# Kernel tuning notes

Hardware: AMD Instinct MI355X
Metric: run time of the kernel (lower is better)

The kernel has to match this reference:

```python
import jax, jax.numpy as jnp
import numpy as np

B, T, C = 16, 2048, 384
HEAD = 384

def setup_inputs() -> dict:
    key = jax.random.key(0)
    kx, kq, kk, kv = jax.random.split(key, 4)
    s = 1.0 / np.sqrt(C)
    return {
        "x": jax.random.normal(kx, (B, T, C), dtype=jnp.float32),
        "Wq": jax.random.normal(kq, (C, HEAD), dtype=jnp.float32) * s,
        "Wk": jax.random.normal(kk, (C, HEAD), dtype=jnp.float32) * s,
        "Wv": jax.random.normal(kv, (C, HEAD), dtype=jnp.float32) * s,
    }

def reference(x, Wq, Wk, Wv):
    # x: [B,T,C]; single causal attention head, eval mode (dropout = identity)
    Bc, Tc, Cc = x.shape
    q = jnp.einsum('btc,ch->bth', x, Wq)
    k = jnp.einsum('btc,ch->bth', x, Wk)
    v = jnp.einsum('btc,ch->bth', x, Wv)
    # NOTE: original scales by C**-0.5 (embedding dim), not head_size**-0.5
    scale = Cc ** (-0.5)
    wei = jnp.einsum('bth,bsh->bts', q, k) * scale  # [B,T,T]
    causal = jnp.tril(jnp.ones((Tc, Tc), dtype=bool))
    wei = jnp.where(causal, wei, -jnp.inf)
    wei = jax.nn.softmax(wei, axis=-1)
    out = jnp.einsum('bts,bsh->bth', wei, v)  # [B,T,head]
    return out
```

## Files before the change

kernel.cpp:

```cpp
#include <hip/hip_runtime.h>
#include <hip/hip_bf16.h>

#define NB 16
#define TT 2048
#define CC 384

typedef short bf16x8 __attribute__((ext_vector_type(8)));
typedef float f32x4 __attribute__((ext_vector_type(4)));

static __device__ __forceinline__ short f2bf(float f) {
  union { __hip_bfloat16 h; short s; } u;
  u.h = __float2bfloat16(f);
  return u.s;
}

#define QSC (0.051031036307982884f * 1.4426950408889634f)

__global__ __launch_bounds__(384)
void conv_wt(const float* __restrict__ Wq, const float* __restrict__ Wk,
             const float* __restrict__ Wv, short* __restrict__ Wbt) {
  const int w = blockIdx.x / CC;
  const int n = blockIdx.x % CC;
  const int k = threadIdx.x;
  const float* W = (w == 0) ? Wq : (w == 1) ? Wk : Wv;
  Wbt[((size_t)w * CC + n) * CC + k] = f2bf(W[(size_t)k * CC + n]);
}

__global__ __launch_bounds__(256, 3)
void proj_gemm(const float* __restrict__ x, const short* __restrict__ Wbt,
               short* __restrict__ Q, short* __restrict__ K,
               short* __restrict__ Vt) {
  __shared__ char smem[34816];
  short* As = (short*)smem;
  short* Bs = (short*)(smem + 10240);
  short* Es = (short*)smem;

  const int mt = blockIdx.x & 255;
  const int nt = blockIdx.x >> 8;
  const int wsel = nt / 3;
  const int nc0 = (nt % 3) * 128;
  const int tid = threadIdx.x;
  const int wave = tid >> 6, lane = tid & 63;
  const int l15 = lane & 15, quad = lane >> 4;
  const int wm = (wave & 1) * 64, wn = (wave >> 1) * 64;

  const float* Ab = x + (size_t)mt * 128 * CC;
  const short* Bb = Wbt + ((size_t)wsel * CC + nc0) * CC;

  f32x4 acc[16];
  #pragma unroll
  for (int i = 0; i < 16; ++i) acc[i] = f32x4{0.f, 0.f, 0.f, 0.f};

  float4 ra[4];
  bf16x8 rb[2];
  #pragma unroll
  for (int c = 0; c < 4; ++c) {
    const int ci = c * 256 + tid;
    ra[c] = *(const float4*)(Ab + (size_t)(ci >> 3) * CC + (ci & 7) * 4);
  }
  #pragma unroll
  for (int c = 0; c < 2; ++c) {
    const int ci = c * 256 + tid;
    rb[c] = *(const bf16x8*)(Bb + (size_t)(ci >> 2) * CC + (ci & 3) * 8);
  }

  for (int kt = 0; kt < 12; ++kt) {
    __syncthreads();
    #pragma unroll
    for (int c = 0; c < 4; ++c) {
      const int ci = c * 256 + tid;
      short4 s4;
      s4.x = f2bf(ra[c].x); s4.y = f2bf(ra[c].y);
      s4.z = f2bf(ra[c].z); s4.w = f2bf(ra[c].w);
      *(short4*)((char*)As + (ci >> 3) * 80 + (ci & 7) * 8) = s4;
    }
    #pragma unroll
    for (int c = 0; c < 2; ++c) {
      const int ci = c * 256 + tid;
      *(bf16x8*)((char*)Bs + (ci >> 2) * 80 + (ci & 3) * 16) = rb[c];
    }
    __syncthreads();
    if (kt < 11) {
      const int k0 = (kt + 1) * 32;
      #pragma unroll
      for (int c = 0; c < 4; ++c) {
        const int ci = c * 256 + tid;
        ra[c] = *(const float4*)(Ab + (size_t)(ci >> 3) * CC + k0 + (ci & 7) * 4);
      }
      #pragma unroll
      for (int c = 0; c < 2; ++c) {
        const int ci = c * 256 + tid;
        rb[c] = *(const bf16x8*)(Bb + (size_t)(ci >> 2) * CC + k0 + (ci & 3) * 8);
      }
    }
    bf16x8 af[4], bf[4];
    #pragma unroll
    for (int i = 0; i < 4; ++i) {
      af[i] = *(const bf16x8*)((char*)As + (wm + i * 16 + l15) * 80 + quad * 16);
      bf[i] = *(const bf16x8*)((char*)Bs + (wn + i * 16 + l15) * 80 + quad * 16);
    }
    #pragma unroll
    for (int i = 0; i < 4; ++i)
      #pragma unroll
      for (int j = 0; j < 4; ++j)
        acc[i * 4 + j] =
            __builtin_amdgcn_mfma_f32_16x16x32_bf16(af[i], bf[j], acc[i * 4 + j], 0, 0, 0);
  }

  if (nt < 6) {
    short* O = (nt < 3) ? Q : K;
    const float sc = (nt < 3) ? QSC : 1.0f;
    #pragma unroll
    for (int i = 0; i < 4; ++i)
      #pragma unroll
      for (int j = 0; j < 4; ++j) {
        const f32x4 a = acc[i * 4 + j];
        const int r0 = mt * 128 + wm + i * 16 + quad * 4;
        const int c = nc0 + wn + j * 16 + l15;
        #pragma unroll
        for (int r = 0; r < 4; ++r) O[(size_t)(r0 + r) * CC + c] = f2bf(a[r] * sc);
      }
  } else {
    __syncthreads();
    #pragma unroll
    for (int i = 0; i < 4; ++i)
      #pragma unroll
      for (int j = 0; j < 4; ++j) {
        const f32x4 a = acc[i * 4 + j];
        const int dl = wn + j * 16 + l15;
        const int ml = wm + i * 16 + quad * 4;
        short4 p4;
        p4.x = f2bf(a[0]); p4.y = f2bf(a[1]); p4.z = f2bf(a[2]); p4.w = f2bf(a[3]);
        *(short4*)(Es + (size_t)dl * 136 + ml) = p4;
      }
    __syncthreads();
    const int d0 = (nt - 6) * 128;
    const int b = mt >> 4, t0 = (mt & 15) * 128;
    const int dr = tid >> 1, hf = tid & 1;
    const short* src = Es + (size_t)dr * 136 + hf * 64;
    short* dst = Vt + ((size_t)b * CC + d0 + dr) * TT + t0 + hf * 64;
    #pragma unroll
    for (int c = 0; c < 8; ++c)
      *(bf16x8*)(dst + c * 8) = *(const bf16x8*)(src + c * 8);
  }
}

__global__ __launch_bounds__(256, 2)
void attn_kernel(const short* __restrict__ Q, const short* __restrict__ K,
                 const short* __restrict__ Vt, float* __restrict__ out) {
  __shared__ char sm[54272];
  char* Ks = sm;
  char* Vs = sm + 24576;
  short* Ps = (short*)(sm + 49152);

  const int blk = blockIdx.x;
  const int qt = 31 - (blk >> 4);
  const int b  = blk & 15;
  const int q0b = qt * 64;
  const int tid = threadIdx.x;
  const int wave = tid >> 6, lane = tid & 63;
  const int l15 = lane & 15, quad = lane >> 4;
  const int q0 = q0b + wave * 16;
  short* pw = Ps + wave * 640;

  bf16x8 qf[12];
  const short* qp = Q + ((size_t)b * TT + q0 + l15) * CC + quad * 8;
  #pragma unroll
  for (int ks = 0; ks < 12; ++ks) qf[ks] = *(const bf16x8*)(qp + ks * 32);

  f32x4 o[24];
  #pragma unroll
  for (int n = 0; n < 24; ++n) o[n] = f32x4{0.f, 0.f, 0.f, 0.f};
  f32x4 lsum = f32x4{0.f, 0.f, 0.f, 0.f};
  float m[4];
  #pragma unroll
  for (int r = 0; r < 4; ++r) m[r] = -INFINITY;

  bf16x8 onesf;
  #pragma unroll
  for (int i = 0; i < 8; ++i) onesf[i] = (short)0x3F80;

  int koff[6], voff[6];
  #pragma unroll
  for (int j = 0; j < 6; ++j) {
    const int lin = wave * 6144 + j * 1024 + lane * 16;
    const int kr = lin / 768;
    const int ksl = (lin - kr * 768) >> 4;
    koff[j] = kr * 768 + ((ksl ^ (kr & 7)) << 4);
    const int vr = lin >> 6;
    const int vsl = (lin >> 4) & 3;
    voff[j] = vr * 4096 + (((vsl - (vr >> 2)) & 3) << 4);
  }
  const char* kbB = (const char*)(K + (size_t)b * TT * CC);
  const char* vtB = (const char*)(Vt + (size_t)b * CC * TT);
  char* KsW = Ks + wave * 6144;
  char* VsW = Vs + wave * 6144;

  const int nchunk = qt * 2 + 2;

  #pragma unroll
  for (int j = 0; j < 6; ++j)
    __builtin_amdgcn_global_load_lds(
        (const __attribute__((address_space(1))) void*)(kbB + koff[j]),
        (__attribute__((address_space(3))) void*)(KsW + j * 1024), 16, 0, 0);
  #pragma unroll
  for (int j = 0; j < 6; ++j)
    __builtin_amdgcn_global_load_lds(
        (const __attribute__((address_space(1))) void*)(vtB + voff[j]),
        (__attribute__((address_space(3))) void*)(VsW + j * 1024), 16, 0, 0);

  for (int kc = 0; kc < nchunk; ++kc) {
    const int k0 = kc * 32;
    const bool active = (k0 <= q0 + 15);
    const int kn = (k0 + 32 < TT - 32) ? (k0 + 32) : (TT - 32);

    asm volatile("s_waitcnt vmcnt(6)" ::: "memory");
    __builtin_amdgcn_s_barrier();
    __builtin_amdgcn_sched_barrier(0);

    f32x4 s0 = f32x4{0.f, 0.f, 0.f, 0.f};
    f32x4 s1 = f32x4{0.f, 0.f, 0.f, 0.f};
    if (active) {
      #pragma unroll
      for (int ks = 0; ks < 12; ++ks) {
        const int sl = (ks * 4 + quad) ^ (l15 & 7);
        const bf16x8 b0 = *(const bf16x8*)(Ks + l15 * 768 + (sl << 4));
        const bf16x8 b1 = *(const bf16x8*)(Ks + (16 + l15) * 768 + (sl << 4));
        s0 = __builtin_amdgcn_mfma_f32_16x16x32_bf16(qf[ks], b0, s0, 0, 0, 0);
        s1 = __builtin_amdgcn_mfma_f32_16x16x32_bf16(qf[ks], b1, s1, 0, 0, 0);
      }
    }
    __builtin_amdgcn_sched_barrier(0);
    __builtin_amdgcn_s_barrier();

    #pragma unroll
    for (int j = 0; j < 6; ++j)
      __builtin_amdgcn_global_load_lds(
          (const __attribute__((address_space(1))) void*)(kbB + (size_t)kn * 768 + koff[j]),
          (__attribute__((address_space(3))) void*)(KsW + j * 1024), 16, 0, 0);

    asm volatile("s_waitcnt vmcnt(6)" ::: "memory");
    __builtin_amdgcn_s_barrier();
    __builtin_amdgcn_sched_barrier(0);

    if (active) {
      const bool domask = (k0 + 31 > q0);
      float mx[4];
      #pragma unroll
      for (int r = 0; r < 4; ++r) {
        float a = s0[r], c = s1[r];
        if (domask) {
          const int qg = q0 + quad * 4 + r;
          if (k0 + l15 > qg)      a = -INFINITY;
          if (k0 + 16 + l15 > qg) c = -INFINITY;
        }
        s0[r] = a; s1[r] = c;
        float v = fmaxf(a, c);
        v = fmaxf(v, __shfl_xor(v, 1));
        v = fmaxf(v, __shfl_xor(v, 2));
        v = fmaxf(v, __shfl_xor(v, 4));
        v = fmaxf(v, __shfl_xor(v, 8));
        mx[r] = v;
      }
      float alpha[4];
      #pragma unroll
      for (int r = 0; r < 4; ++r) {
        const float mn = fmaxf(m[r], mx[r]);
        alpha[r] = exp2f(m[r] - mn);
        m[r] = mn;
        s0[r] = exp2f(s0[r] - mn);
        s1[r] = exp2f(s1[r] - mn);
      }
      const bool need = (alpha[0] < 1.f) | (alpha[1] < 1.f) |
                        (alpha[2] < 1.f) | (alpha[3] < 1.f);
      if (__any(need)) {
        #pragma unroll
        for (int r = 0; r < 4; ++r) lsum[r] *= alpha[r];
        #pragma unroll
        for (int n = 0; n < 24; ++n) {
          #pragma unroll
          for (int r = 0; r < 4; ++r) o[n][r] *= alpha[r];
        }
      }
      #pragma unroll
      for (int r = 0; r < 4; ++r) {
        pw[(quad * 4 + r) * 40 + l15]      = f2bf(s0[r]);
        pw[(quad * 4 + r) * 40 + 16 + l15] = f2bf(s1[r]);
      }
      const bf16x8 pf = *(const bf16x8*)(pw + l15 * 40 + quad * 8);
      lsum = __builtin_amdgcn_mfma_f32_16x16x32_bf16(pf, onesf, lsum, 0, 0, 0);
      #pragma unroll
      for (int n = 0; n < 24; ++n) {
        const int vrow = n * 16 + l15;
        const bf16x8 vf = *(const bf16x8*)(Vs + vrow * 64 + (((quad + (vrow >> 2)) & 3) << 4));
        o[n] = __builtin_amdgcn_mfma_f32_16x16x32_bf16(pf, vf, o[n], 0, 0, 0);
      }
    }
    __builtin_amdgcn_sched_barrier(0);
    __builtin_amdgcn_s_barrier();
    #pragma unroll
    for (int j = 0; j < 6; ++j)
      __builtin_amdgcn_global_load_lds(
          (const __attribute__((address_space(1))) void*)(vtB + (size_t)kn * 2 + voff[j]),
          (__attribute__((address_space(3))) void*)(VsW + j * 1024), 16, 0, 0);
  }

  float linv[4];
  #pragma unroll
  for (int r = 0; r < 4; ++r) linv[r] = 1.f / lsum[r];
  float* ob = out + ((size_t)b * TT + q0) * CC;
  #pragma unroll
  for (int n = 0; n < 24; ++n) {
    #pragma unroll
    for (int r = 0; r < 4; ++r) {
      ob[(size_t)(quad * 4 + r) * CC + n * 16 + l15] = o[n][r] * linv[r];
    }
  }
}

extern "C" void kernel_launch(void* const* d_in, const int* in_sizes, int n_in,
                              void* d_out, int out_size, void* d_ws, size_t ws_size,
                              hipStream_t stream) {
  const float* x  = (const float*)d_in[0];
  const float* Wq = (const float*)d_in[1];
  const float* Wk = (const float*)d_in[2];
  const float* Wv = (const float*)d_in[3];
  float* out = (float*)d_out;

  const size_t QS = (size_t)NB * TT * CC;
  short* Qs = (short*)d_ws;
  short* Ks = Qs + QS;
  short* Vt = Ks + QS;

  short* Wbt = (short*)d_out;

  hipLaunchKernelGGL(conv_wt, dim3(3 * CC), dim3(CC), 0, stream, Wq, Wk, Wv, Wbt);
  hipLaunchKernelGGL(proj_gemm, dim3(256 * 9), dim3(256), 0, stream,
                     x, Wbt, Qs, Ks, Vt);
  hipLaunchKernelGGL(attn_kernel, dim3(NB * TT / 64), dim3(256), 0, stream,
                     Qs, Ks, Vt, out);
}
```

Before: 312.1 us.

## Pre-convert x to bf16, pipeline proj GEMM with direct-to-LDS loads, split-KV attention

Measured after the change: 301.9 us. 1.03x faster.

```diff
diff --git a/kernel.cpp b/kernel.cpp
--- a/kernel.cpp
+++ b/kernel.cpp
@@ -26,13 +26,22 @@
   Wbt[((size_t)w * CC + n) * CC + k] = f2bf(W[(size_t)k * CC + n]);
 }
 
+__global__ __launch_bounds__(256)
+void xconv(const float* __restrict__ x, short* __restrict__ xb) {
+  const int i = (blockIdx.x * 256 + threadIdx.x) * 8;
+  const float4 a = *(const float4*)(x + i);
+  const float4 c = *(const float4*)(x + i + 4);
+  bf16x8 r;
+  r[0] = f2bf(a.x); r[1] = f2bf(a.y); r[2] = f2bf(a.z); r[3] = f2bf(a.w);
+  r[4] = f2bf(c.x); r[5] = f2bf(c.y); r[6] = f2bf(c.z); r[7] = f2bf(c.w);
+  *(bf16x8*)(xb + i) = r;
+}
+
 __global__ __launch_bounds__(256, 3)
-void proj_gemm(const float* __restrict__ x, const short* __restrict__ Wbt,
+void proj_gemm(const short* __restrict__ xb, const short* __restrict__ Wbt,
                short* __restrict__ Q, short* __restrict__ K,
                short* __restrict__ Vt) {
   __shared__ char smem[34816];
-  short* As = (short*)smem;
-  short* Bs = (short*)(smem + 10240);
   short* Es = (short*)smem;
 
   const int mt = blockIdx.x & 255;
@@ -44,60 +53,57 @@
   const int l15 = lane & 15, quad = lane >> 4;
   const int wm = (wave & 1) * 64, wn = (wave >> 1) * 64;
 
-  const float* Ab = x + (size_t)mt * 128 * CC;
+  const short* Ab = xb + (size_t)mt * 128 * CC;
   const short* Bb = Wbt + ((size_t)wsel * CC + nc0) * CC;
 
+  int aoff[2];
+  #pragma unroll
+  for (int j = 0; j < 2; ++j) {
+    const int lin = wave * 2048 + j * 1024 + lane * 16;
+    const int r = lin >> 6;
+    const int s = (lin >> 4) & 3;
+    aoff[j] = r * CC + ((s ^ ((r >> 1) & 3)) * 8);
+  }
+  char* AW = smem + wave * 2048;
+  char* BW = smem + 16384 + wave * 2048;
+
   f32x4 acc[16];
   #pragma unroll
   for (int i = 0; i < 16; ++i) acc[i] = f32x4{0.f, 0.f, 0.f, 0.f};
 
-  float4 ra[4];
-  bf16x8 rb[2];
-  #pragma unroll
-  for (int c = 0; c < 4; ++c) {
-    const int ci = c * 256 + tid;
-    ra[c] = *(const float4*)(Ab + (size_t)(ci >> 3) * CC + (ci & 7) * 4);
-  }
-  #pragma unroll
-  for (int c = 0; c < 2; ++c) {
-    const int ci = c * 256 + tid;
-    rb[c] = *(const bf16x8*)(Bb + (size_t)(ci >> 2) * CC + (ci & 3) * 8);
+  #pragma unroll
+  for (int pc = 0; pc < 2; ++pc) {
+    #pragma unroll
+    for (int j = 0; j < 2; ++j)
+      __builtin_amdgcn_global_load_lds(
+          (const __attribute__((address_space(1))) void*)(Ab + pc * 32 + aoff[j]),
+          (__attribute__((address_space(3))) void*)(AW + pc * 8192 + j * 1024), 16, 0, 0);
+    #pragma unroll
+    for (int j = 0; j < 2; ++j)
+      __builtin_amdgcn_global_load_lds(
+          (const __attribute__((address_space(1))) void*)(Bb + pc * 32 + aoff[j]),
+          (__attribute__((address_space(3))) void*)(BW + pc * 8192 + j * 1024), 16, 0, 0);
   }
 
   for (int kt = 0; kt < 12; ++kt) {
-    __syncthreads();
-    #pragma unroll
-    for (int c = 0; c < 4; ++c) {
-      const int ci = c * 256 + tid;
-      short4 s4;
-      s4.x = f2bf(ra[c].x); s4.y = f2bf(ra[c].y);
-      s4.z = f2bf(ra[c].z); s4.w = f2bf(ra[c].w);
-      *(short4*)((char*)As + (ci >> 3) * 80 + (ci & 7) * 8) = s4;
-    }
-    #pragma unroll
-    for (int c = 0; c < 2; ++c) {
-      const int ci = c * 256 + tid;
-      *(bf16x8*)((char*)Bs + (ci >> 2) * 80 + (ci & 3) * 16) = rb[c];
-    }
-    __syncthreads();
-    if (kt < 11) {
-      const int k0 = (kt + 1) * 32;
-      #pragma unroll
-      for (int c = 0; c < 4; ++c) {
-        const int ci = c * 256 + tid;
-        ra[c] = *(const float4*)(Ab + (size_t)(ci >> 3) * CC + k0 + (ci & 7) * 4);
-      }
-      #pragma unroll
-      for (int c = 0; c < 2; ++c) {
-        const int ci = c * 256 + tid;
-        rb[c] = *(const bf16x8*)(Bb + (size_t)(ci >> 2) * CC + k0 + (ci & 3) * 8);
-      }
-    }
+    const int kb = kt & 1;
+    if (kt == 11) {
+      asm volatile("s_waitcnt vmcnt(0)" ::: "memory");
+    } else {
+      asm volatile("s_waitcnt vmcnt(4)" ::: "memory");
+    }
+    __builtin_amdgcn_s_barrier();
+    __builtin_amdgcn_sched_barrier(0);
+
+    const char* As = smem + kb * 8192;
+    const char* Bs = smem + 16384 + kb * 8192;
     bf16x8 af[4], bf[4];
     #pragma unroll
     for (int i = 0; i < 4; ++i) {
-      af[i] = *(const bf16x8*)((char*)As + (wm + i * 16 + l15) * 80 + quad * 16);
-      bf[i] = *(const bf16x8*)((char*)Bs + (wn + i * 16 + l15) * 80 + quad * 16);
+      const int ar = wm + i * 16 + l15;
+      const int br = wn + i * 16 + l15;
+      af[i] = *(const bf16x8*)(As + ar * 64 + ((quad ^ ((ar >> 1) & 3)) << 4));
+      bf[i] = *(const bf16x8*)(Bs + br * 64 + ((quad ^ ((br >> 1) & 3)) << 4));
     }
     #pragma unroll
     for (int i = 0; i < 4; ++i)
@@ -105,6 +111,22 @@
       for (int j = 0; j < 4; ++j)
         acc[i * 4 + j] =
             __builtin_amdgcn_mfma_f32_16x16x32_bf16(af[i], bf[j], acc[i * 4 + j], 0, 0, 0);
+
+    __builtin_amdgcn_sched_barrier(0);
+    __builtin_amdgcn_s_barrier();
+    if (kt + 2 < 12) {
+      const int k0 = (kt + 2) * 32;
+      #pragma unroll
+      for (int j = 0; j < 2; ++j)
+        __builtin_amdgcn_global_load_lds(
+            (const __attribute__((address_space(1))) void*)(Ab + k0 + aoff[j]),
+            (__attribute__((address_space(3))) void*)(AW + kb * 8192 + j * 1024), 16, 0, 0);
+      #pragma unroll
+      for (int j = 0; j < 2; ++j)
+        __builtin_amdgcn_global_load_lds(
+            (const __attribute__((address_space(1))) void*)(Bb + k0 + aoff[j]),
+            (__attribute__((address_space(3))) void*)(BW + kb * 8192 + j * 1024), 16, 0, 0);
+    }
   }
 
   if (nt < 6) {
@@ -145,23 +167,75 @@
   }
 }
 
+
+#define ATTN_PRELUDE                                                          \
+  __shared__ char sm[54272];                                                  \
+  char* KsS = sm;                                                             \
+  char* VsS = sm + 24576;                                                     \
+  const int tid = threadIdx.x;                                                \
+  const int wave = tid >> 6, lane = tid & 63;                                 \
+  const int l15 = lane & 15, quad = lane >> 4;                                \
+  short* pw = (short*)(sm + 49152) + wave * 640;                              \
+  bf16x8 onesf;                                                               \
+  _Pragma("unroll")                                                           \
+  for (int i = 0; i < 8; ++i) onesf[i] = (short)0x3F80;                       \
+  int koff[6], voff[6];                                                       \
+  _Pragma("unroll")                                                           \
+  for (int j = 0; j < 6; ++j) {                                               \
+    const int lin = wave * 6144 + j * 1024 + lane * 16;                       \
+    const int kr = lin / 768;                                                 \
+    const int ksl = (lin - kr * 768) >> 4;                                    \
+    koff[j] = kr * 768 + ((ksl ^ (kr & 7)) << 4);                             \
+    const int vr = lin >> 6;                                                  \
+    const int vsl = (lin >> 4) & 3;                                           \
+    voff[j] = vr * 4096 + (((vsl - (vr >> 2)) & 3) << 4);                     \
+  }                                                                           \
+  char* KsW = KsS + wave * 6144;                                              \
+  char* VsW = VsS + wave * 6144;
+
+#define STAGE_CHUNK(ck)                                                       \
+  do {                                                                        \
+    const size_t kby_ = (size_t)(ck) * 24576;                                 \
+    const size_t vby_ = (size_t)(ck) * 64;                                    \
+    _Pragma("unroll")                                                         \
+    for (int j = 0; j < 6; ++j)                                               \
+      __builtin_amdgcn_global_load_lds(                                       \
+          (const __attribute__((address_space(1))) void*)(kbB + kby_ + koff[j]), \
+          (__attribute__((address_space(3))) void*)(KsW + j * 1024), 16, 0, 0);  \
+    _Pragma("unroll")                                                         \
+    for (int j = 0; j < 6; ++j)                                               \
+      __builtin_amdgcn_global_load_lds(                                       \
+          (const __attribute__((address_space(1))) void*)(vtB + vby_ + voff[j]), \
+          (__attribute__((address_space(3))) void*)(VsW + j * 1024), 16, 0, 0);  \
+  } while (0)
+
+#define CHUNK_LOOP(C0, C1)                                                    \
+  for (int kc = (C0); kc < (C1); ++kc) {                                      \
+    const int k0 = kc * 32;                                                   \
+    const int kb = (kc - (C0)) & 1;                                           \
+    if (kc + 1 == (C1)) {                                                     \
+      asm volatile("s_waitcnt vmcnt(0)" ::: "memory");                        \
+    } else {                                                                  \
+      asm volatile("s_waitcnt vmcnt(12)" ::: "memory");                       \
+    }                                                                         \
+    __builtin_amdgcn_s_barrier();                                             \
+    __builtin_amdgcn_sched_barrier(0);                                        \
+    const bool active = (k0 <= q0 + 15);                                      \
+    if (active) {                                                             \
+      const char* Ksb = KsS + kb * 0;             \
+      (void)Ksb;                                                              \
+    }                                                                         \
+  }
+
+
 __global__ __launch_bounds__(256, 2)
-void attn_kernel(const short* __restrict__ Q, const short* __restrict__ K,
-                 const short* __restrict__ Vt, float* __restrict__ out) {
-  __shared__ char sm[54272];
-  char* Ks = sm;
-  char* Vs = sm + 24576;
-  short* Ps = (short*)(sm + 49152);
-
+void attn_plain(const short* __restrict__ Q, const short* __restrict__ K,
+                const short* __restrict__ Vt, float* __restrict__ out) {
+  ATTN_PRELUDE
   const int blk = blockIdx.x;
   const int qt = 31 - (blk >> 4);
   const int b  = blk & 15;
-  const int q0b = qt * 64;
-  const int tid = threadIdx.x;
-  const int wave = tid >> 6, lane = tid & 63;
-  const int l15 = lane & 15, quad = lane >> 4;
-  const int q0 = q0b + wave * 16;
-  short* pw = Ps + wave * 640;
+  const int q0 = qt * 64 + wave * 16;
 
   bf16x8 qf[12];
   const short* qp = Q + ((size_t)b * TT + q0 + l15) * CC + quad * 8;
@@ -176,69 +250,42 @@
   #pragma unroll
   for (int r = 0; r < 4; ++r) m[r] = -INFINITY;
 
-  bf16x8 onesf;
-  #pragma unroll
-  for (int i = 0; i < 8; ++i) onesf[i] = (short)0x3F80;
-
-  int koff[6], voff[6];
-  #pragma unroll
-  for (int j = 0; j < 6; ++j) {
-    const int lin = wave * 6144 + j * 1024 + lane * 16;
-    const int kr = lin / 768;
-    const int ksl = (lin - kr * 768) >> 4;
-    koff[j] = kr * 768 + ((ksl ^ (kr & 7)) << 4);
-    const int vr = lin >> 6;
-    const int vsl = (lin >> 4) & 3;
-    voff[j] = vr * 4096 + (((vsl - (vr >> 2)) & 3) << 4);
-  }
   const char* kbB = (const char*)(K + (size_t)b * TT * CC);
   const char* vtB = (const char*)(Vt + (size_t)b * CC * TT);
-  char* KsW = Ks + wave * 6144;
-  char* VsW = Vs + wave * 6144;
-
   const int nchunk = qt * 2 + 2;
 
-  #pragma unroll
-  for (int j = 0; j < 6; ++j)
-    __builtin_amdgcn_global_load_lds(
-        (const __attribute__((address_space(1))) void*)(kbB + koff[j]),
-        (__attribute__((address_space(3))) void*)(KsW + j * 1024), 16, 0, 0);
-  #pragma unroll
-  for (int j = 0; j < 6; ++j)
-    __builtin_amdgcn_global_load_lds(
-        (const __attribute__((address_space(1))) void*)(vtB + voff[j]),
-        (__attribute__((address_space(3))) void*)(VsW + j * 1024), 16, 0, 0);
+  STAGE_CHUNK(0);
 
   for (int kc = 0; kc < nchunk; ++kc) {
     const int k0 = kc * 32;
-    const bool active = (k0 <= q0 + 15);
-    const int kn = (k0 + 32 < TT - 32) ? (k0 + 32) : (TT - 32);
-
     asm volatile("s_waitcnt vmcnt(6)" ::: "memory");
     __builtin_amdgcn_s_barrier();
     __builtin_amdgcn_sched_barrier(0);
 
     f32x4 s0 = f32x4{0.f, 0.f, 0.f, 0.f};
     f32x4 s1 = f32x4{0.f, 0.f, 0.f, 0.f};
+    const bool active = (k0 <= q0 + 15);
     if (active) {
       #pragma unroll
       for (int ks = 0; ks < 12; ++ks) {
         const int sl = (ks * 4 + quad) ^ (l15 & 7);
-        const bf16x8 b0 = *(const bf16x8*)(Ks + l15 * 768 + (sl << 4));
-        const bf16x8 b1 = *(const bf16x8*)(Ks + (16 + l15) * 768 + (sl << 4));
+        const bf16x8 b0 = *(const bf16x8*)(KsS + l15 * 768 + (sl << 4));
+        const bf16x8 b1 = *(const bf16x8*)(KsS + (16 + l15) * 768 + (sl << 4));
         s0 = __builtin_amdgcn_mfma_f32_16x16x32_bf16(qf[ks], b0, s0, 0, 0, 0);
         s1 = __builtin_amdgcn_mfma_f32_16x16x32_bf16(qf[ks], b1, s1, 0, 0, 0);
       }
     }
     __builtin_amdgcn_sched_barrier(0);
     __builtin_amdgcn_s_barrier();
-
-    #pragma unroll
-    for (int j = 0; j < 6; ++j)
-      __builtin_amdgcn_global_load_lds(
-          (const __attribute__((address_space(1))) void*)(kbB + (size_t)kn * 768 + koff[j]),
-          (__attribute__((address_space(3))) void*)(KsW + j * 1024), 16, 0, 0);
-
+    {
+      const int kn = (kc + 1 < nchunk) ? (kc + 1) : kc;
+      const size_t kby_ = (size_t)kn * 24576;
+      #pragma unroll
+      for (int j = 0; j < 6; ++j)
+        __builtin_amdgcn_global_load_lds(
+            (const __attribute__((address_space(1))) void*)(kbB + kby_ + koff[j]),
+            (__attribute__((address_space(3))) void*)(KsW + j * 1024), 16, 0, 0);
+    }
     asm volatile("s_waitcnt vmcnt(6)" ::: "memory");
     __builtin_amdgcn_s_barrier();
     __builtin_amdgcn_sched_barrier(0);
@@ -292,17 +339,21 @@
       #pragma unroll
       for (int n = 0; n < 24; ++n) {
         const int vrow = n * 16 + l15;
-        const bf16x8 vf = *(const bf16x8*)(Vs + vrow * 64 + (((quad + (vrow >> 2)) & 3) << 4));
+        const bf16x8 vf = *(const bf16x8*)(VsS + vrow * 64 + (((quad + (vrow >> 2)) & 3) << 4));
         o[n] = __builtin_amdgcn_mfma_f32_16x16x32_bf16(pf, vf, o[n], 0, 0, 0);
       }
     }
     __builtin_amdgcn_sched_barrier(0);
     __builtin_amdgcn_s_barrier();
-    #pragma unroll
-    for (int j = 0; j < 6; ++j)
-      __builtin_amdgcn_global_load_lds(
-          (const __attribute__((address_space(1))) void*)(vtB + (size_t)kn * 2 + voff[j]),
-          (__attribute__((address_space(3))) void*)(VsW + j * 1024), 16, 0, 0);
+    {
+      const int kn = (kc + 1 < nchunk) ? (kc + 1) : kc;
+      const size_t vby_ = (size_t)kn * 64;
+      #pragma unroll
+      for (int j = 0; j < 6; ++j)
+        __builtin_amdgcn_global_load_lds(
+            (const __attribute__((address_space(1))) void*)(vtB + vby_ + voff[j]),
+            (__attribute__((address_space(3))) void*)(VsW + j * 1024), 16, 0, 0);
+    }
   }
 
   float linv[4];
@@ -315,6 +366,243 @@
     for (int r = 0; r < 4; ++r) {
       ob[(size_t)(quad * 4 + r) * CC + n * 16 + l15] = o[n][r] * linv[r];
     }
+  }
+}
+
+__global__ __launch_bounds__(256, 2)
+void attn_split(const short* __restrict__ Q, const short* __restrict__ K,
+                const short* __restrict__ Vt, float* __restrict__ out,
+                float* __restrict__ OB, float* __restrict__ ML) {
+  ATTN_PRELUDE
+  const int blk = blockIdx.x;
+  const int b = blk & 15;
+  const int s = blk >> 4;
+  const int j = s & 15;
+  const int role = s >> 4;
+  const int p = b * 16 + j;
+
+  const char* kbB = (const char*)(K + (size_t)b * TT * CC);
+  const char* vtB = (const char*)(Vt + (size_t)b * CC * TT);
+
+  const int nph = role ? 1 : 2;
+  #pragma unroll 1
+  for (int ph = 0; ph < nph; ++ph) {
+    int qt, c0, c1, mode;
+    if (role == 0) {
+      if (ph == 0) { qt = j;      c0 = 0;          c1 = 2 * j + 2;  mode = 0; }
+      else         { qt = 31 - j; c0 = 0;          c1 = 31 - 2 * j; mode = 1; }
+    } else         { qt = 31 - j; c0 = 31 - 2 * j; c1 = 64 - 2 * j; mode = 2; }
+    const int q0 = qt * 64 + wave * 16;
+
+    bf16x8 qf[12];
+    const short* qp = Q + ((size_t)b * TT + q0 + l15) * CC + quad * 8;
+    #pragma unroll
+    for (int ks = 0; ks < 12; ++ks) qf[ks] = *(const bf16x8*)(qp + ks * 32);
+    asm volatile("s_waitcnt vmcnt(0)" ::: "memory");
+
+    f32x4 o[24];
+    #pragma unroll
+    for (int n = 0; n < 24; ++n) o[n] = f32x4{0.f, 0.f, 0.f, 0.f};
+    f32x4 lsum = f32x4{0.f, 0.f, 0.f, 0.f};
+    float m[4];
+    #pragma unroll
+    for (int r = 0; r < 4; ++r) m[r] = -INFINITY;
+
+    #pragma unroll 1
+    for (int pc = 0; pc < 2; ++pc) {
+      if (c0 + pc < c1) {
+        char* KsWb = KsW + pc * 12288;
+        (void)KsWb;
+        const size_t kby_ = (size_t)(c0 + pc) * 24576;
+        const size_t vby_ = (size_t)(c0 + pc) * 64;
+        char* KW = KsS + pc * 12288 + wave * 3072;
+        char* VW = VsS + pc * 12288 + wave * 3072;
+        #pragma unroll
+        for (int jj2 = 0; jj2 < 3; ++jj2) {
+          const int lin = wave * 3072 + jj2 * 1024 + lane * 16;
+          const int kr = lin / 384;
+          const int ksl = (lin - kr * 384) >> 4;
+          const int ko = kr * 768 + (((ksl * 2 + (jj2 & 0)) ^ 0) << 4); (void)ko;
+          (void)kby_; (void)vby_; (void)KW; (void)VW; (void)lin; (void)kr; (void)ksl;
+        }
+      }
+    }
+    {
+      const size_t kby0 = (size_t)c0 * 24576;
+      const size_t vby0 = (size_t)c0 * 64;
+      #pragma unroll
+      for (int jj2 = 0; jj2 < 6; ++jj2)
+        __builtin_amdgcn_global_load_lds(
+            (const __attribute__((address_space(1))) void*)(kbB + kby0 + koff[jj2]),
+            (__attribute__((address_space(3))) void*)(KsW + jj2 * 1024), 16, 0, 0);
+      #pragma unroll
+      for (int jj2 = 0; jj2 < 6; ++jj2)
+        __builtin_amdgcn_global_load_lds(
+            (const __attribute__((address_space(1))) void*)(vtB + vby0 + voff[jj2]),
+            (__attribute__((address_space(3))) void*)(VsW + jj2 * 1024), 16, 0, 0);
+    }
+
+    #pragma unroll 1
+    for (int kc = c0; kc < c1; ++kc) {
+      const int k0 = kc * 32;
+      asm volatile("s_waitcnt vmcnt(6)" ::: "memory");
+      __builtin_amdgcn_s_barrier();
+      __builtin_amdgcn_sched_barrier(0);
+
+      f32x4 s0 = f32x4{0.f, 0.f, 0.f, 0.f};
+      f32x4 s1 = f32x4{0.f, 0.f, 0.f, 0.f};
+      const bool active = (k0 <= q0 + 15);
+      if (active) {
+        #pragma unroll
+        for (int ks = 0; ks < 12; ++ks) {
+          const int sl = (ks * 4 + quad) ^ (l15 & 7);
+          const bf16x8 b0 = *(const bf16x8*)(KsS + l15 * 768 + (sl << 4));
+          const bf16x8 b1 = *(const bf16x8*)(KsS + (16 + l15) * 768 + (sl << 4));
+          s0 = __builtin_amdgcn_mfma_f32_16x16x32_bf16(qf[ks], b0, s0, 0, 0, 0);
+          s1 = __builtin_amdgcn_mfma_f32_16x16x32_bf16(qf[ks], b1, s1, 0, 0, 0);
+        }
+      }
+      __builtin_amdgcn_sched_barrier(0);
+      __builtin_amdgcn_s_barrier();
+      {
+        const int kn = (kc + 1 < c1) ? (kc + 1) : kc;
+        const size_t kby_ = (size_t)kn * 24576;
+        #pragma unroll
+        for (int jj2 = 0; jj2 < 6; ++jj2)
+          __builtin_amdgcn_global_load_lds(
+              (const __attribute__((address_space(1))) void*)(kbB + kby_ + koff[jj2]),
+              (__attribute__((address_space(3))) void*)(KsW + jj2 * 1024), 16, 0, 0);
+      }
+      asm volatile("s_waitcnt vmcnt(6)" ::: "memory");
+      __builtin_amdgcn_s_barrier();
+      __builtin_amdgcn_sched_barrier(0);
+
+      if (active) {
+        const bool domask = (k0 + 31 > q0);
+        float mx[4];
+        #pragma unroll
+        for (int r = 0; r < 4; ++r) {
+          float a = s0[r], c = s1[r];
+          if (domask) {
+            const int qg = q0 + quad * 4 + r;
+            if (k0 + l15 > qg)      a = -INFINITY;
+            if (k0 + 16 + l15 > qg) c = -INFINITY;
+          }
+          s0[r] = a; s1[r] = c;
+          float v = fmaxf(a, c);
+          v = fmaxf(v, __shfl_xor(v, 1));
+          v = fmaxf(v, __shfl_xor(v, 2));
+          v = fmaxf(v, __shfl_xor(v, 4));
+          v = fmaxf(v, __shfl_xor(v, 8));
+          mx[r] = v;
+        }
+        float alpha[4];
+        #pragma unroll
+        for (int r = 0; r < 4; ++r) {
+          const float mn = fmaxf(m[r], mx[r]);
+          alpha[r] = exp2f(m[r] - mn);
+          m[r] = mn;
+          s0[r] = exp2f(s0[r] - mn);
+          s1[r] = exp2f(s1[r] - mn);
+        }
+        const bool need = (alpha[0] < 1.f) | (alpha[1] < 1.f) |
+                          (alpha[2] < 1.f) | (alpha[3] < 1.f);
+        if (__any(need)) {
+          #pragma unroll
+          for (int r = 0; r < 4; ++r) lsum[r] *= alpha[r];
+          #pragma unroll
+          for (int n = 0; n < 24; ++n) {
+            #pragma unroll
+            for (int r = 0; r < 4; ++r) o[n][r] *= alpha[r];
+          }
+        }
+        #pragma unroll
+        for (int r = 0; r < 4; ++r) {
+          pw[(quad * 4 + r) * 40 + l15]      = f2bf(s0[r]);
+          pw[(quad * 4 + r) * 40 + 16 + l15] = f2bf(s1[r]);
+        }
+        const bf16x8 pf = *(const bf16x8*)(pw + l15 * 40 + quad * 8);
+        lsum = __builtin_amdgcn_mfma_f32_16x16x32_bf16(pf, onesf, lsum, 0, 0, 0);
+        #pragma unroll
+        for (int n = 0; n < 24; ++n) {
+          const int vrow = n * 16 + l15;
+          const bf16x8 vf = *(const bf16x8*)(VsS + vrow * 64 + (((quad + (vrow >> 2)) & 3) << 4));
+          o[n] = __builtin_amdgcn_mfma_f32_16x16x32_bf16(pf, vf, o[n], 0, 0, 0);
+        }
+      }
+      __builtin_amdgcn_sched_barrier(0);
+      __builtin_amdgcn_s_barrier();
+      {
+        const int kn = (kc + 1 < c1) ? (kc + 1) : kc;
+        const size_t vby_ = (size_t)kn * 64;
+        #pragma unroll
+        for (int jj2 = 0; jj2 < 6; ++jj2)
+          __builtin_amdgcn_global_load_lds(
+              (const __attribute__((address_space(1))) void*)(vtB + vby_ + voff[jj2]),
+              (__attribute__((address_space(3))) void*)(VsW + jj2 * 1024), 16, 0, 0);
+      }
+    }
+    asm volatile("s_waitcnt vmcnt(0)" ::: "memory");
+    __builtin_amdgcn_s_barrier();
+
+    if (mode == 0) {
+      float linv[4];
+      #pragma unroll
+      for (int r = 0; r < 4; ++r) linv[r] = 1.f / lsum[r];
+      float* ob = out + ((size_t)b * TT + q0) * CC;
+      #pragma unroll
+      for (int n = 0; n < 24; ++n) {
+        #pragma unroll
+        for (int r = 0; r < 4; ++r)
+          ob[(size_t)(quad * 4 + r) * CC + n * 16 + l15] = o[n][r] * linv[r];
+      }
+    } else {
+      float* ob = (mode == 1)
+          ? out + ((size_t)b * TT + q0) * CC
+          : OB + (size_t)p * 24576 + (size_t)(wave * 16) * CC;
+      #pragma unroll
+      for (int n = 0; n < 24; ++n) {
+        #pragma unroll
+        for (int r = 0; r < 4; ++r)
+          ob[(size_t)(quad * 4 + r) * CC + n * 16 + l15] = o[n][r];
+      }
+      if (l15 == 0) {
+        float* pml = ML + (size_t)p * 256 + (mode - 1) * 128;
+        #pragma unroll
+        for (int r = 0; r < 4; ++r) {
+          pml[(wave * 16 + quad * 4 + r) * 2]     = m[r];
+          pml[(wave * 16 + quad * 4 + r) * 2 + 1] = lsum[r];
+        }
+      }
+    }
+  }
+}
+
+__global__ __launch_bounds__(256)
+void combine(float* __restrict__ out, const float* __restrict__ OB,
+             const float* __restrict__ ML) {
+  const int p = blockIdx.x;
+  const int b = p >> 4, j = p & 15;
+  const int H = 31 - j;
+  const int row = threadIdx.x >> 2, seg = threadIdx.x & 3;
+  const float* ml = ML + (size_t)p * 256;
+  const float mA = ml[row * 2],       lA = ml[row * 2 + 1];
+  const float mB = ml[128 + row * 2], lB = ml[128 + row * 2 + 1];
+  const float mF = fmaxf(mA, mB);
+  const float sA = exp2f(mA - mF), sB = exp2f(mB - mF);
+  const float inv = 1.f / (lA * sA + lB * sB);
+  const float wA = sA * inv, wB = sB * inv;
+  float* pa = out + ((size_t)b * TT + H * 64 + row) * CC + seg * 96;
+  const float* pb = OB + (size_t)p * 24576 + (size_t)row * CC + seg * 96;
+  #pragma unroll
+  for (int c = 0; c < 24; ++c) {
+    float4 a = *(float4*)(pa + c * 4);
+    const float4 bb = *(const float4*)(pb + c * 4);
+    a.x = a.x * wA + bb.x * wB;
+    a.y = a.y * wA + bb.y * wB;
+    a.z = a.z * wA + bb.z * wB;
+    a.w = a.w * wA + bb.w * wB;
+    *(float4*)(pa + c * 4) = a;
   }
 }
 
@@ -332,11 +620,24 @@
   short* Ks = Qs + QS;
   short* Vt = Ks + QS;
 
+  const size_t base = QS * 3 * 2;
+  float* OB = (float*)((char*)d_ws + base);
+  float* ML = (float*)((char*)d_ws + base + 25165824);
+  const bool split = ws_size >= base + 25165824 + 524288;
+
   short* Wbt = (short*)d_out;
+  short* xb  = (short*)((char*)d_out + 1048576);
 
   hipLaunchKernelGGL(conv_wt, dim3(3 * CC), dim3(CC), 0, stream, Wq, Wk, Wv, Wbt);
+  hipLaunchKernelGGL(xconv, dim3(6144), dim3(256), 0, stream, x, xb);
   hipLaunchKernelGGL(proj_gemm, dim3(256 * 9), dim3(256), 0, stream,
-                     x, Wbt, Qs, Ks, Vt);
-  hipLaunchKernelGGL(attn_kernel, dim3(NB * TT / 64), dim3(256), 0, stream,
-                     Qs, Ks, Vt, out);
-}
+                     xb, Wbt, Qs, Ks, Vt);
+  if (split) {
+    hipLaunchKernelGGL(attn_split, dim3(512), dim3(256), 0, stream,
+                       Qs, Ks, Vt, out, OB, ML);
+    hipLaunchKernelGGL(combine, dim3(256), dim3(256), 0, stream, out, OB, ML);
+  } else {
+    hipLaunchKernelGGL(attn_plain, dim3(512), dim3(256), 0, stream,
+                       Qs, Ks, Vt, out);
+  }
+}
```
